# Optimization experiments

Hardware: AMD Instinct MI355X
Metric: run time of the kernel (lower is better)

## Reference

```python
import jax, jax.numpy as jnp
import numpy as np

HIDDEN = 896
N_HEADS = 14
N_KV = 2
HEAD_DIM = HIDDEN // N_HEADS  # 64
N_REP = N_HEADS // N_KV       # 7
ROPE_THETA = 1000000.0


def setup_inputs() -> dict:
    key = jax.random.key(0)
    ks = jax.random.split(key, 8)
    B, S = 2, 2048
    s = 0.02
    return {
        "hidden_states": jax.random.normal(ks[0], (B, S, HIDDEN), dtype=jnp.float32),
        "position_ids": jnp.broadcast_to(jnp.arange(S, dtype=jnp.int64), (B, S)),
        "Wq": jax.random.normal(ks[1], (HIDDEN, HIDDEN), dtype=jnp.float32) * s,
        "bq": jnp.zeros((HIDDEN,), dtype=jnp.float32),
        "Wk": jax.random.normal(ks[2], (N_KV * HEAD_DIM, HIDDEN), dtype=jnp.float32) * s,
        "bk": jnp.zeros((N_KV * HEAD_DIM,), dtype=jnp.float32),
        "Wv": jax.random.normal(ks[3], (N_KV * HEAD_DIM, HIDDEN), dtype=jnp.float32) * s,
        "bv": jnp.zeros((N_KV * HEAD_DIM,), dtype=jnp.float32),
        "Wo": jax.random.normal(ks[4], (HIDDEN, HIDDEN), dtype=jnp.float32) * s,
    }


def _rotate_half(x):
    x1, x2 = x[..., : HEAD_DIM // 2], x[..., HEAD_DIM // 2 :]
    return jnp.concatenate((-x2, x1), axis=-1)


def reference(hidden_states, position_ids, Wq, bq, Wk, bk, Wv, bv, Wo):
    B, S, _ = hidden_states.shape
    q = (hidden_states @ Wq.T + bq).reshape(B, S, N_HEADS, HEAD_DIM)
    k = (hidden_states @ Wk.T + bk).reshape(B, S, N_KV, HEAD_DIM)
    v = (hidden_states @ Wv.T + bv).reshape(B, S, N_KV, HEAD_DIM)

    # RoPE: cos/sin [B, S, 1, HEAD_DIM]
    inv_freq = 1.0 / (ROPE_THETA ** (jnp.arange(0, HEAD_DIM, 2, dtype=jnp.float32) / HEAD_DIM))
    freqs = position_ids.astype(jnp.float32)[..., None] * inv_freq  # [B,S,D/2]
    emb = jnp.concatenate((freqs, freqs), axis=-1)
    cos = jnp.cos(emb)[:, :, None, :]
    sin = jnp.sin(emb)[:, :, None, :]
    q = q * cos + _rotate_half(q) * sin
    k = k * cos + _rotate_half(k) * sin

    # [B, H, S, D]; repeat KV heads (GQA)
    q = q.transpose(0, 2, 1, 3)
    k = jnp.repeat(k.transpose(0, 2, 1, 3), N_REP, axis=1)
    v = jnp.repeat(v.transpose(0, 2, 1, 3), N_REP, axis=1)

    scale = 1.0 / np.sqrt(HEAD_DIM)
    scores = jnp.einsum("bhqd,bhkd->bhqk", q, k) * scale
    causal = jnp.tril(jnp.ones((S, S), dtype=bool))
    scores = jnp.where(causal[None, None, :, :], scores, jnp.finfo(scores.dtype).min)
    probs = jax.nn.softmax(scores, axis=-1)
    attn = jnp.einsum("bhqk,bhkd->bhqd", probs, v)  # [B,H,S,D]
    attn = attn.transpose(0, 2, 1, 3).reshape(B, S, HIDDEN)
    return attn @ Wo.T
```

## Files before the change

kernel.cpp:

```cpp
#include <hip/hip_runtime.h>

#define HID 896
#define NH 14
#define NKV 2
#define NREP 7
#define SEQ 2048
#define BT 2
#define NTOK (BT*SEQ)
#define CSCALE 0.18033688011112042f

typedef __attribute__((ext_vector_type(8))) short bf16x8;
typedef __attribute__((ext_vector_type(8))) unsigned short u16x8;
typedef __attribute__((ext_vector_type(4))) float fx4;
typedef __attribute__((ext_vector_type(4))) short s16x4;
typedef _Float16 f16x4 __attribute__((ext_vector_type(4)));

__device__ __forceinline__ unsigned short f2b(float x){
  union { float f; unsigned u; } a; a.f = x;
  unsigned r = a.u + 0x7FFFu + ((a.u >> 16) & 1u);
  return (unsigned short)(r >> 16);
}
__device__ __forceinline__ unsigned short f2h(float x){
  union { _Float16 h; unsigned short u; } a; a.h = (_Float16)x; return a.u;
}

__global__ __launch_bounds__(256) void qkv_rope_kernel(
    const float* __restrict__ hidden, const int* __restrict__ pos,
    const float* __restrict__ Wq, const float* __restrict__ bq,
    const float* __restrict__ Wk, const float* __restrict__ bk,
    const float* __restrict__ Wv, const float* __restrict__ bv,
    unsigned short* __restrict__ qo, unsigned short* __restrict__ ko,
    unsigned short* __restrict__ vt)
{
  __shared__ short As[64*40];
  __shared__ short Bs[64*40];
  const int tid = threadIdx.x;
  const int bm = blockIdx.x, bn = blockIdx.y;
  const int w = tid >> 6, l = tid & 63, l15 = l & 15, l16 = l >> 4;

  const float *W, *bias; int kind, hloc;
  if (bn < NH)      { W = Wq + (size_t)bn*64*HID;      bias = bq + bn*64;      kind = 0; hloc = bn; }
  else if (bn < 16) { W = Wk + (size_t)(bn-NH)*64*HID; bias = bk + (bn-NH)*64; kind = 1; hloc = bn-NH; }
  else              { W = Wv + (size_t)(bn-16)*64*HID; bias = bv + (bn-16)*64; kind = 2; hloc = bn-16; }

  fx4 acc[4] = {{0,0,0,0},{0,0,0,0},{0,0,0,0},{0,0,0,0}};

  const int r = tid >> 2, c8 = (tid & 3) * 8;
  const float* ap0 = hidden + (size_t)(bm*64 + r)*HID + c8;
  const float* bp0 = W + (size_t)r*HID + c8;

  for (int kc = 0; kc < HID; kc += 32){
    __syncthreads();
    float4 a0 = *(const float4*)(ap0 + kc);
    float4 a1 = *(const float4*)(ap0 + kc + 4);
    float4 b0 = *(const float4*)(bp0 + kc);
    float4 b1 = *(const float4*)(bp0 + kc + 4);
    bf16x8 avv, bvv;
    avv[0]=(short)f2b(a0.x); avv[1]=(short)f2b(a0.y); avv[2]=(short)f2b(a0.z); avv[3]=(short)f2b(a0.w);
    avv[4]=(short)f2b(a1.x); avv[5]=(short)f2b(a1.y); avv[6]=(short)f2b(a1.z); avv[7]=(short)f2b(a1.w);
    bvv[0]=(short)f2b(b0.x); bvv[1]=(short)f2b(b0.y); bvv[2]=(short)f2b(b0.z); bvv[3]=(short)f2b(b0.w);
    bvv[4]=(short)f2b(b1.x); bvv[5]=(short)f2b(b1.y); bvv[6]=(short)f2b(b1.z); bvv[7]=(short)f2b(b1.w);
    *(bf16x8*)&As[r*40 + c8] = avv;
    *(bf16x8*)&Bs[r*40 + c8] = bvv;
    __syncthreads();
    bf16x8 af = *(bf16x8*)&As[(w*16 + l15)*40 + l16*8];
#pragma unroll
    for (int nt = 0; nt < 4; nt++){
      bf16x8 bfr = *(bf16x8*)&Bs[(nt*16 + l15)*40 + l16*8];
      acc[nt] = __builtin_amdgcn_mfma_f32_16x16x32_bf16(af, bfr, acc[nt], 0, 0, 0);
    }
  }

  float bl[4];
#pragma unroll
  for (int nt = 0; nt < 4; nt++) bl[nt] = bias[nt*16 + l15];

  if (kind == 2){
#pragma unroll
    for (int j = 0; j < 4; j++){
      int grow = bm*64 + w*16 + l16*4 + j;
      int b = grow >> 11, s = grow & (SEQ-1);
      int tile = s >> 6, key = s & 63;
      unsigned short* dst = vt + (size_t)(((b*NKV + hloc)*(SEQ/64) + tile)*4096);
#pragma unroll
      for (int nt = 0; nt < 4; nt++)
        dst[(nt*16 + l15)*64 + key] = f2h(acc[nt][j] + bl[nt]);
    }
  } else {
    float invf[2];
#pragma unroll
    for (int nt = 0; nt < 2; nt++)
      invf[nt] = exp2f(-(float)(nt*16 + l15) * 0.62286151779138041f);
#pragma unroll
    for (int j = 0; j < 4; j++){
      int grow = bm*64 + w*16 + l16*4 + j;
      int b = grow >> 11, s = grow & (SEQ-1);
      float p = (float)pos[grow];
      unsigned short* dst = (kind == 0)
          ? qo + ((size_t)(b*NH  + hloc)*SEQ + s)*64
          : ko + ((size_t)(b*NKV + hloc)*SEQ + s)*64;
#pragma unroll
      for (int nt = 0; nt < 2; nt++){
        int d = nt*16 + l15;
        float f = p * invf[nt];
        float sv, cv;
        sincosf(f, &sv, &cv);
        float x1 = acc[nt][j]   + bl[nt];
        float x2 = acc[nt+2][j] + bl[nt+2];
        dst[d]    = f2b(x1*cv - x2*sv);
        dst[d+32] = f2b(x2*cv + x1*sv);
      }
    }
  }
}

__device__ __forceinline__ void smax_pv(
    const fx4* s, bool diag, int wl , int q4,
    float& m_run, float& l_run, fx4* o, const f16x4 vf[4][4])
{
  float tv[16];
#pragma unroll
  for (int tl = 0; tl < 4; tl++)
#pragma unroll
    for (int j = 0; j < 4; j++){
      float x = s[tl][j]*CSCALE;
      if (diag && (tl*16 + q4*4 + j > wl)) x = -1e30f;
      tv[tl*4+j] = x;
    }
  float mx = tv[0];
#pragma unroll
  for (int i = 1; i < 16; i++) mx = fmaxf(mx, tv[i]);
  mx = fmaxf(mx, __shfl_xor(mx, 16));
  mx = fmaxf(mx, __shfl_xor(mx, 32));
  float mn = fmaxf(m_run, mx);
  float al = exp2f(m_run - mn);
  m_run = mn;
  float p[16], rs = 0.f;
#pragma unroll
  for (int i = 0; i < 16; i++){ p[i] = exp2f(tv[i] - mn); rs += p[i]; }
  rs += __shfl_xor(rs, 16);
  rs += __shfl_xor(rs, 32);
  l_run = l_run*al + rs;
#pragma unroll
  for (int nt = 0; nt < 4; nt++)
#pragma unroll
    for (int j = 0; j < 4; j++) o[nt][j] *= al;
  f16x4 pf[4];
#pragma unroll
  for (int tl = 0; tl < 4; tl++){
    pf[tl][0] = (_Float16)p[tl*4+0];
    pf[tl][1] = (_Float16)p[tl*4+1];
    pf[tl][2] = (_Float16)p[tl*4+2];
    pf[tl][3] = (_Float16)p[tl*4+3];
  }
#pragma unroll
  for (int nt = 0; nt < 4; nt++)
#pragma unroll
    for (int tl = 0; tl < 4; tl++)
      o[nt] = __builtin_amdgcn_mfma_f32_16x16x16f16(vf[nt][tl], pf[tl], o[nt], 0,0,0);
}

__global__ __launch_bounds__(256) void attn_kernel(
    const unsigned short* __restrict__ q, const unsigned short* __restrict__ k,
    const unsigned short* __restrict__ vt, unsigned short* __restrict__ ao)
{
  __shared__ short Ks[64*72];
  __shared__ short Vt[64*72];

  const int tid = threadIdx.x;
  const int w = tid >> 6, l = tid & 63, l15 = l & 15, q4 = l >> 4;
  const int tlo = blockIdx.x, thi = 31 - tlo;
  const int h = blockIdx.y, b = blockIdx.z, kvh = h / NREP;
  const int wl = w*16 + l15;

  const unsigned short* qbase = q + ((size_t)(b*NH + h)*SEQ)*64;
  const unsigned short* qpA = qbase + (size_t)(thi*64 + wl)*64;
  const unsigned short* qpB = qbase + (size_t)(tlo*64 + wl)*64;
  bf16x8 qA0 = *(const bf16x8*)(qpA + q4*8), qA1 = *(const bf16x8*)(qpA + 32 + q4*8);
  bf16x8 qB0 = *(const bf16x8*)(qpB + q4*8), qB1 = *(const bf16x8*)(qpB + 32 + q4*8);

  fx4 oA[4] = {{0,0,0,0},{0,0,0,0},{0,0,0,0},{0,0,0,0}};
  fx4 oB[4] = {{0,0,0,0},{0,0,0,0},{0,0,0,0},{0,0,0,0}};
  float mA = -1e30f, lA = 0.f, mB = -1e30f, lB = 0.f;

  const unsigned short* kbase = k  + ((size_t)(b*NKV + kvh)*SEQ)*64;
  const unsigned short* vbase = vt + (size_t)((b*NKV + kvh)*(SEQ/64))*4096;

  u16x8 kreg[2], vreg[2];
#pragma unroll
  for (int p = 0; p < 2; p++){
    int n = p*256 + tid;
    kreg[p] = *(const u16x8*)(kbase + n*8);
    vreg[p] = *(const u16x8*)(vbase + n*8);
  }

  for (int kt = 0; kt <= thi; kt++){
#pragma unroll
    for (int p = 0; p < 2; p++){
      int n = p*256 + tid, rr = n >> 3, g = n & 7;
      *(u16x8*)&Ks[rr*72 + g*8] = kreg[p];
      *(u16x8*)&Vt[rr*72 + g*8] = vreg[p];
    }
    __syncthreads();

    if (kt < thi){
      const unsigned short* kn = kbase + (size_t)(kt+1)*4096;
      const unsigned short* vn = vbase + (size_t)(kt+1)*4096;
#pragma unroll
      for (int p = 0; p < 2; p++){
        int n = p*256 + tid;
        kreg[p] = *(const u16x8*)(kn + n*8);
        vreg[p] = *(const u16x8*)(vn + n*8);
      }
    }

    bf16x8 kf0[4], kf1[4];
#pragma unroll
    for (int tl = 0; tl < 4; tl++){
      kf0[tl] = *(bf16x8*)&Ks[(tl*16 + l15)*72 + q4*8];
      kf1[tl] = *(bf16x8*)&Ks[(tl*16 + l15)*72 + 32 + q4*8];
    }
    f16x4 vf[4][4];
#pragma unroll
    for (int nt = 0; nt < 4; nt++)
#pragma unroll
      for (int tl = 0; tl < 4; tl++)
        vf[nt][tl] = *(f16x4*)&Vt[(nt*16 + l15)*72 + tl*16 + q4*4];

    {
      fx4 s[4] = {{0,0,0,0},{0,0,0,0},{0,0,0,0},{0,0,0,0}};
#pragma unroll
      for (int tl = 0; tl < 4; tl++){
        s[tl] = __builtin_amdgcn_mfma_f32_16x16x32_bf16(kf0[tl], qA0, s[tl], 0,0,0);
        s[tl] = __builtin_amdgcn_mfma_f32_16x16x32_bf16(kf1[tl], qA1, s[tl], 0,0,0);
      }
      smax_pv(s, kt == thi, wl, q4, mA, lA, oA, vf);
    }
    if (kt <= tlo){
      fx4 s[4] = {{0,0,0,0},{0,0,0,0},{0,0,0,0},{0,0,0,0}};
#pragma unroll
      for (int tl = 0; tl < 4; tl++){
        s[tl] = __builtin_amdgcn_mfma_f32_16x16x32_bf16(kf0[tl], qB0, s[tl], 0,0,0);
        s[tl] = __builtin_amdgcn_mfma_f32_16x16x32_bf16(kf1[tl], qB1, s[tl], 0,0,0);
      }
      smax_pv(s, kt == tlo, wl, q4, mB, lB, oB, vf);
    }
    __syncthreads();
  }

  {
    float inv = 1.0f / lA;
    unsigned short* dst = ao + ((size_t)(b*SEQ + thi*64 + wl))*HID + h*64;
#pragma unroll
    for (int nt = 0; nt < 4; nt++){
      s16x4 ov;
      ov[0] = (short)f2b(oA[nt][0]*inv); ov[1] = (short)f2b(oA[nt][1]*inv);
      ov[2] = (short)f2b(oA[nt][2]*inv); ov[3] = (short)f2b(oA[nt][3]*inv);
      *(s16x4*)(dst + nt*16 + q4*4) = ov;
    }
  }
  {
    float inv = 1.0f / lB;
    unsigned short* dst = ao + ((size_t)(b*SEQ + tlo*64 + wl))*HID + h*64;
#pragma unroll
    for (int nt = 0; nt < 4; nt++){
      s16x4 ov;
      ov[0] = (short)f2b(oB[nt][0]*inv); ov[1] = (short)f2b(oB[nt][1]*inv);
      ov[2] = (short)f2b(oB[nt][2]*inv); ov[3] = (short)f2b(oB[nt][3]*inv);
      *(s16x4*)(dst + nt*16 + q4*4) = ov;
    }
  }
}

__global__ __launch_bounds__(256) void out_gemm_kernel(
    const unsigned short* __restrict__ A, const float* __restrict__ Wo,
    float* __restrict__ out)
{
  __shared__ short As[64*40];
  __shared__ short Bs[64*40];
  const int tid = threadIdx.x;
  const int bm = blockIdx.x, bn = blockIdx.y;
  const int w = tid >> 6, l = tid & 63, l15 = l & 15, l16 = l >> 4;

  fx4 acc[4] = {{0,0,0,0},{0,0,0,0},{0,0,0,0},{0,0,0,0}};
  const int r = tid >> 2, c8 = (tid & 3)*8;
  const unsigned short* ap0 = A + (size_t)(bm*64 + r)*HID + c8;
  const float* bp0 = Wo + (size_t)(bn*64 + r)*HID + c8;

  for (int kc = 0; kc < HID; kc += 32){
    __syncthreads();
    u16x8 a8 = *(const u16x8*)(ap0 + kc);
    float4 b0 = *(const float4*)(bp0 + kc);
    float4 b1 = *(const float4*)(bp0 + kc + 4);
    bf16x8 bvv;
    bvv[0]=(short)f2b(b0.x); bvv[1]=(short)f2b(b0.y); bvv[2]=(short)f2b(b0.z); bvv[3]=(short)f2b(b0.w);
    bvv[4]=(short)f2b(b1.x); bvv[5]=(short)f2b(b1.y); bvv[6]=(short)f2b(b1.z); bvv[7]=(short)f2b(b1.w);
    *(u16x8*)&As[r*40 + c8] = a8;
    *(bf16x8*)&Bs[r*40 + c8] = bvv;
    __syncthreads();
    bf16x8 af = *(bf16x8*)&As[(w*16 + l15)*40 + l16*8];
#pragma unroll
    for (int nt = 0; nt < 4; nt++){
      bf16x8 bfr = *(bf16x8*)&Bs[(nt*16 + l15)*40 + l16*8];
      acc[nt] = __builtin_amdgcn_mfma_f32_16x16x32_bf16(af, bfr, acc[nt], 0, 0, 0);
    }
  }

#pragma unroll
  for (int j = 0; j < 4; j++){
    int grow = bm*64 + w*16 + l16*4 + j;
    float* dst = out + (size_t)grow*HID + bn*64;
#pragma unroll
    for (int nt = 0; nt < 4; nt++)
      dst[nt*16 + l15] = acc[nt][j];
  }
}

extern "C" void kernel_launch(void* const* d_in, const int* in_sizes, int n_in,
                              void* d_out, int out_size, void* d_ws, size_t ws_size,
                              hipStream_t stream)
{
  const float* hidden = (const float*)d_in[0];
  const int*   pos    = (const int*)d_in[1];
  const float* Wq = (const float*)d_in[2]; const float* bq = (const float*)d_in[3];
  const float* Wk = (const float*)d_in[4]; const float* bk = (const float*)d_in[5];
  const float* Wv = (const float*)d_in[6]; const float* bv = (const float*)d_in[7];
  const float* Wo = (const float*)d_in[8];

  unsigned short* qws  = (unsigned short*)d_ws;
  unsigned short* kws  = qws + (size_t)BT*NH*SEQ*64;
  unsigned short* vtws = kws + (size_t)BT*NKV*SEQ*64;
  unsigned short* aws  = vtws + (size_t)BT*NKV*SEQ*64;

  qkv_rope_kernel<<<dim3(NTOK/64, 18), 256, 0, stream>>>(
      hidden, pos, Wq, bq, Wk, bk, Wv, bv, qws, kws, vtws);
  attn_kernel<<<dim3(16, NH, BT), 256, 0, stream>>>(qws, kws, vtws, aws);
  out_gemm_kernel<<<dim3(NTOK/64, NH), 256, 0, stream>>>(aws, Wo, (float*)d_out);
}
```

Measured before the change: 186.6 us.

## Pre-convert inputs to bf16 and use 128x128 register-prefetched GEMM tiles

A new conversion kernel turns hidden states and all weights into bf16 once, so the GEMM inner loops no longer repeat the fp32-to-bf16 conversion for every tile. The QKV and output GEMMs move from 64x64 to 128x128 tiles with a 64-wide K step. Each wave now computes a 4x4 grid of MFMA blocks, and the next K tile is prefetched into registers while the current one is computed. The attention output reuses the bf16 hidden-state buffer. In exchange there is an extra kernel launch and extra traffic to write the converted tensors, and the larger tiles leave fewer blocks in the grid, which lowers occupancy.

```diff
diff --git a/kernel.cpp b/kernel.cpp
--- a/kernel.cpp
+++ b/kernel.cpp
@@ -24,98 +24,147 @@
   union { _Float16 h; unsigned short u; } a; a.h = (_Float16)x; return a.u;
 }
 
-__global__ __launch_bounds__(256) void qkv_rope_kernel(
-    const float* __restrict__ hidden, const int* __restrict__ pos,
-    const float* __restrict__ Wq, const float* __restrict__ bq,
-    const float* __restrict__ Wk, const float* __restrict__ bk,
-    const float* __restrict__ Wv, const float* __restrict__ bv,
+__global__ __launch_bounds__(256) void cvt_kernel(
+    const float* __restrict__ s0, const float* __restrict__ s1,
+    const float* __restrict__ s2, const float* __restrict__ s3,
+    const float* __restrict__ s4,
+    unsigned short* __restrict__ d0, unsigned short* __restrict__ d1,
+    unsigned short* __restrict__ d2, unsigned short* __restrict__ d3,
+    unsigned short* __restrict__ d4,
+    int c0, int c1, int c2, int c3, int c4)
+{
+  const float* s; unsigned short* d; int c;
+  switch (blockIdx.y){
+    case 0: s=s0; d=d0; c=c0; break;
+    case 1: s=s1; d=d1; c=c1; break;
+    case 2: s=s2; d=d2; c=c2; break;
+    case 3: s=s3; d=d3; c=c3; break;
+    default: s=s4; d=d4; c=c4; break;
+  }
+  for (int i = (blockIdx.x*256 + threadIdx.x)*8; i < c; i += gridDim.x*2048){
+    float4 a = *(const float4*)(s + i);
+    float4 b = *(const float4*)(s + i + 4);
+    u16x8 o;
+    o[0]=f2b(a.x); o[1]=f2b(a.y); o[2]=f2b(a.z); o[3]=f2b(a.w);
+    o[4]=f2b(b.x); o[5]=f2b(b.y); o[6]=f2b(b.z); o[7]=f2b(b.w);
+    *(u16x8*)(d + i) = o;
+  }
+}
+
+__global__ __launch_bounds__(256) void qkv_gemm_kernel(
+    const unsigned short* __restrict__ A, const unsigned short* __restrict__ Bw,
+    const float* __restrict__ bq, const float* __restrict__ bk, const float* __restrict__ bv,
+    const int* __restrict__ pos,
     unsigned short* __restrict__ qo, unsigned short* __restrict__ ko,
     unsigned short* __restrict__ vt)
 {
-  __shared__ short As[64*40];
-  __shared__ short Bs[64*40];
+  __shared__ short As[128*72];
+  __shared__ short Bs[128*72];
   const int tid = threadIdx.x;
   const int bm = blockIdx.x, bn = blockIdx.y;
-  const int w = tid >> 6, l = tid & 63, l15 = l & 15, l16 = l >> 4;
-
-  const float *W, *bias; int kind, hloc;
-  if (bn < NH)      { W = Wq + (size_t)bn*64*HID;      bias = bq + bn*64;      kind = 0; hloc = bn; }
-  else if (bn < 16) { W = Wk + (size_t)(bn-NH)*64*HID; bias = bk + (bn-NH)*64; kind = 1; hloc = bn-NH; }
-  else              { W = Wv + (size_t)(bn-16)*64*HID; bias = bv + (bn-16)*64; kind = 2; hloc = bn-16; }
-
-  fx4 acc[4] = {{0,0,0,0},{0,0,0,0},{0,0,0,0},{0,0,0,0}};
-
-  const int r = tid >> 2, c8 = (tid & 3) * 8;
-  const float* ap0 = hidden + (size_t)(bm*64 + r)*HID + c8;
-  const float* bp0 = W + (size_t)r*HID + c8;
-
-  for (int kc = 0; kc < HID; kc += 32){
-    __syncthreads();
-    float4 a0 = *(const float4*)(ap0 + kc);
-    float4 a1 = *(const float4*)(ap0 + kc + 4);
-    float4 b0 = *(const float4*)(bp0 + kc);
-    float4 b1 = *(const float4*)(bp0 + kc + 4);
-    bf16x8 avv, bvv;
-    avv[0]=(short)f2b(a0.x); avv[1]=(short)f2b(a0.y); avv[2]=(short)f2b(a0.z); avv[3]=(short)f2b(a0.w);
-    avv[4]=(short)f2b(a1.x); avv[5]=(short)f2b(a1.y); avv[6]=(short)f2b(a1.z); avv[7]=(short)f2b(a1.w);
-    bvv[0]=(short)f2b(b0.x); bvv[1]=(short)f2b(b0.y); bvv[2]=(short)f2b(b0.z); bvv[3]=(short)f2b(b0.w);
-    bvv[4]=(short)f2b(b1.x); bvv[5]=(short)f2b(b1.y); bvv[6]=(short)f2b(b1.z); bvv[7]=(short)f2b(b1.w);
-    *(bf16x8*)&As[r*40 + c8] = avv;
-    *(bf16x8*)&Bs[r*40 + c8] = bvv;
-    __syncthreads();
-    bf16x8 af = *(bf16x8*)&As[(w*16 + l15)*40 + l16*8];
-#pragma unroll
-    for (int nt = 0; nt < 4; nt++){
-      bf16x8 bfr = *(bf16x8*)&Bs[(nt*16 + l15)*40 + l16*8];
-      acc[nt] = __builtin_amdgcn_mfma_f32_16x16x32_bf16(af, bfr, acc[nt], 0, 0, 0);
-    }
-  }
-
+  const int w = tid >> 6, l = tid & 63, l15 = l & 15, q4 = l >> 4;
+  const int wm = w & 1, wn = w >> 1;
+
+  fx4 acc[4][4] = {};
+
+  const int srow = tid >> 3, scol = (tid & 7)*8;
+  const unsigned short* Ag = A  + (size_t)(bm*128 + srow)*HID + scol;
+  const unsigned short* Bg = Bw + (size_t)(bn*128 + srow)*HID + scol;
+
+  u16x8 ar[4], br[4];
+#pragma unroll
+  for (int p = 0; p < 4; p++){
+    ar[p] = *(const u16x8*)(Ag + (size_t)p*32*HID);
+    br[p] = *(const u16x8*)(Bg + (size_t)p*32*HID);
+  }
+
+  for (int kt = 0; kt < 14; kt++){
+#pragma unroll
+    for (int p = 0; p < 4; p++){
+      *(u16x8*)&As[(srow + p*32)*72 + scol] = ar[p];
+      *(u16x8*)&Bs[(srow + p*32)*72 + scol] = br[p];
+    }
+    __syncthreads();
+    if (kt < 13){
+      const int ko_ = (kt+1)*64;
+#pragma unroll
+      for (int p = 0; p < 4; p++){
+        ar[p] = *(const u16x8*)(Ag + (size_t)p*32*HID + ko_);
+        br[p] = *(const u16x8*)(Bg + (size_t)p*32*HID + ko_);
+      }
+    }
+#pragma unroll
+    for (int ks = 0; ks < 2; ks++){
+      bf16x8 af[4], bf[4];
+#pragma unroll
+      for (int mt = 0; mt < 4; mt++)
+        af[mt] = *(bf16x8*)&As[(wm*64 + mt*16 + l15)*72 + ks*32 + q4*8];
+#pragma unroll
+      for (int nt = 0; nt < 4; nt++)
+        bf[nt] = *(bf16x8*)&Bs[(wn*64 + nt*16 + l15)*72 + ks*32 + q4*8];
+#pragma unroll
+      for (int mt = 0; mt < 4; mt++)
+#pragma unroll
+        for (int nt = 0; nt < 4; nt++)
+          acc[mt][nt] = __builtin_amdgcn_mfma_f32_16x16x32_bf16(af[mt], bf[nt], acc[mt][nt], 0,0,0);
+    }
+    __syncthreads();
+  }
+
+  const int hu = bn*2 + wn;
+  const float* bias; int kind, hloc;
+  if (hu < NH)      { bias = bq + hu*64;      kind = 0; hloc = hu; }
+  else if (hu < 16) { bias = bk + (hu-NH)*64; kind = 1; hloc = hu-NH; }
+  else              { bias = bv + (hu-16)*64; kind = 2; hloc = hu-16; }
   float bl[4];
 #pragma unroll
   for (int nt = 0; nt < 4; nt++) bl[nt] = bias[nt*16 + l15];
 
   if (kind == 2){
 #pragma unroll
-    for (int j = 0; j < 4; j++){
-      int grow = bm*64 + w*16 + l16*4 + j;
-      int b = grow >> 11, s = grow & (SEQ-1);
-      int tile = s >> 6, key = s & 63;
-      unsigned short* dst = vt + (size_t)(((b*NKV + hloc)*(SEQ/64) + tile)*4096);
-#pragma unroll
-      for (int nt = 0; nt < 4; nt++)
-        dst[(nt*16 + l15)*64 + key] = f2h(acc[nt][j] + bl[nt]);
-    }
+    for (int mt = 0; mt < 4; mt++)
+#pragma unroll
+      for (int j = 0; j < 4; j++){
+        int grow = bm*128 + wm*64 + mt*16 + q4*4 + j;
+        int b = grow >> 11, s = grow & (SEQ-1);
+        int tile = s >> 6, key = s & 63;
+        unsigned short* dst = vt + (size_t)(((b*NKV + hloc)*(SEQ/64) + tile)*4096);
+#pragma unroll
+        for (int nt = 0; nt < 4; nt++)
+          dst[(nt*16 + l15)*64 + key] = f2h(acc[mt][nt][j] + bl[nt]);
+      }
   } else {
     float invf[2];
 #pragma unroll
     for (int nt = 0; nt < 2; nt++)
       invf[nt] = exp2f(-(float)(nt*16 + l15) * 0.62286151779138041f);
 #pragma unroll
-    for (int j = 0; j < 4; j++){
-      int grow = bm*64 + w*16 + l16*4 + j;
-      int b = grow >> 11, s = grow & (SEQ-1);
-      float p = (float)pos[grow];
-      unsigned short* dst = (kind == 0)
-          ? qo + ((size_t)(b*NH  + hloc)*SEQ + s)*64
-          : ko + ((size_t)(b*NKV + hloc)*SEQ + s)*64;
-#pragma unroll
-      for (int nt = 0; nt < 2; nt++){
-        int d = nt*16 + l15;
-        float f = p * invf[nt];
-        float sv, cv;
-        sincosf(f, &sv, &cv);
-        float x1 = acc[nt][j]   + bl[nt];
-        float x2 = acc[nt+2][j] + bl[nt+2];
-        dst[d]    = f2b(x1*cv - x2*sv);
-        dst[d+32] = f2b(x2*cv + x1*sv);
-      }
-    }
+    for (int mt = 0; mt < 4; mt++)
+#pragma unroll
+      for (int j = 0; j < 4; j++){
+        int grow = bm*128 + wm*64 + mt*16 + q4*4 + j;
+        int b = grow >> 11, s = grow & (SEQ-1);
+        float p = (float)pos[grow];
+        unsigned short* dst = (kind == 0)
+            ? qo + ((size_t)(b*NH  + hloc)*SEQ + s)*64
+            : ko + ((size_t)(b*NKV + hloc)*SEQ + s)*64;
+#pragma unroll
+        for (int nt = 0; nt < 2; nt++){
+          int d = nt*16 + l15;
+          float f = p * invf[nt];
+          float sv, cv;
+          sincosf(f, &sv, &cv);
+          float x1 = acc[mt][nt][j]   + bl[nt];
+          float x2 = acc[mt][nt+2][j] + bl[nt+2];
+          dst[d]    = f2b(x1*cv - x2*sv);
+          dst[d+32] = f2b(x2*cv + x1*sv);
+        }
+      }
   }
 }
 
 __device__ __forceinline__ void smax_pv(
-    const fx4* s, bool diag, int wl , int q4,
+    const fx4* s, bool diag, int wl, int q4,
     float& m_run, float& l_run, fx4* o, const f16x4 vf[4][4])
 {
   float tv[16];
@@ -273,47 +322,72 @@
 }
 
 __global__ __launch_bounds__(256) void out_gemm_kernel(
-    const unsigned short* __restrict__ A, const float* __restrict__ Wo,
+    const unsigned short* __restrict__ A, const unsigned short* __restrict__ Bw,
     float* __restrict__ out)
 {
-  __shared__ short As[64*40];
-  __shared__ short Bs[64*40];
+  __shared__ short As[128*72];
+  __shared__ short Bs[128*72];
   const int tid = threadIdx.x;
   const int bm = blockIdx.x, bn = blockIdx.y;
-  const int w = tid >> 6, l = tid & 63, l15 = l & 15, l16 = l >> 4;
-
-  fx4 acc[4] = {{0,0,0,0},{0,0,0,0},{0,0,0,0},{0,0,0,0}};
-  const int r = tid >> 2, c8 = (tid & 3)*8;
-  const unsigned short* ap0 = A + (size_t)(bm*64 + r)*HID + c8;
-  const float* bp0 = Wo + (size_t)(bn*64 + r)*HID + c8;
-
-  for (int kc = 0; kc < HID; kc += 32){
-    __syncthreads();
-    u16x8 a8 = *(const u16x8*)(ap0 + kc);
-    float4 b0 = *(const float4*)(bp0 + kc);
-    float4 b1 = *(const float4*)(bp0 + kc + 4);
-    bf16x8 bvv;
-    bvv[0]=(short)f2b(b0.x); bvv[1]=(short)f2b(b0.y); bvv[2]=(short)f2b(b0.z); bvv[3]=(short)f2b(b0.w);
-    bvv[4]=(short)f2b(b1.x); bvv[5]=(short)f2b(b1.y); bvv[6]=(short)f2b(b1.z); bvv[7]=(short)f2b(b1.w);
-    *(u16x8*)&As[r*40 + c8] = a8;
-    *(bf16x8*)&Bs[r*40 + c8] = bvv;
-    __syncthreads();
-    bf16x8 af = *(bf16x8*)&As[(w*16 + l15)*40 + l16*8];
-#pragma unroll
-    for (int nt = 0; nt < 4; nt++){
-      bf16x8 bfr = *(bf16x8*)&Bs[(nt*16 + l15)*40 + l16*8];
-      acc[nt] = __builtin_amdgcn_mfma_f32_16x16x32_bf16(af, bfr, acc[nt], 0, 0, 0);
-    }
-  }
-
-#pragma unroll
-  for (int j = 0; j < 4; j++){
-    int grow = bm*64 + w*16 + l16*4 + j;
-    float* dst = out + (size_t)grow*HID + bn*64;
-#pragma unroll
-    for (int nt = 0; nt < 4; nt++)
-      dst[nt*16 + l15] = acc[nt][j];
-  }
+  const int w = tid >> 6, l = tid & 63, l15 = l & 15, q4 = l >> 4;
+  const int wm = w & 1, wn = w >> 1;
+
+  fx4 acc[4][4] = {};
+
+  const int srow = tid >> 3, scol = (tid & 7)*8;
+  const unsigned short* Ag = A  + (size_t)(bm*128 + srow)*HID + scol;
+  const unsigned short* Bg = Bw + (size_t)(bn*128 + srow)*HID + scol;
+
+  u16x8 ar[4], br[4];
+#pragma unroll
+  for (int p = 0; p < 4; p++){
+    ar[p] = *(const u16x8*)(Ag + (size_t)p*32*HID);
+    br[p] = *(const u16x8*)(Bg + (size_t)p*32*HID);
+  }
+
+  for (int kt = 0; kt < 14; kt++){
+#pragma unroll
+    for (int p = 0; p < 4; p++){
+      *(u16x8*)&As[(srow + p*32)*72 + scol] = ar[p];
+      *(u16x8*)&Bs[(srow + p*32)*72 + scol] = br[p];
+    }
+    __syncthreads();
+    if (kt < 13){
+      const int ko_ = (kt+1)*64;
+#pragma unroll
+      for (int p = 0; p < 4; p++){
+        ar[p] = *(const u16x8*)(Ag + (size_t)p*32*HID + ko_);
+        br[p] = *(const u16x8*)(Bg + (size_t)p*32*HID + ko_);
+      }
+    }
+#pragma unroll
+    for (int ks = 0; ks < 2; ks++){
+      bf16x8 af[4], bf[4];
+#pragma unroll
+      for (int mt = 0; mt < 4; mt++)
+        af[mt] = *(bf16x8*)&As[(wm*64 + mt*16 + l15)*72 + ks*32 + q4*8];
+#pragma unroll
+      for (int nt = 0; nt < 4; nt++)
+        bf[nt] = *(bf16x8*)&Bs[(wn*64 + nt*16 + l15)*72 + ks*32 + q4*8];
+#pragma unroll
+      for (int mt = 0; mt < 4; mt++)
+#pragma unroll
+        for (int nt = 0; nt < 4; nt++)
+          acc[mt][nt] = __builtin_amdgcn_mfma_f32_16x16x32_bf16(af[mt], bf[nt], acc[mt][nt], 0,0,0);
+    }
+    __syncthreads();
+  }
+
+#pragma unroll
+  for (int mt = 0; mt < 4; mt++)
+#pragma unroll
+    for (int j = 0; j < 4; j++){
+      int grow = bm*128 + wm*64 + mt*16 + q4*4 + j;
+      float* dst = out + (size_t)grow*HID + bn*128 + wn*64;
+#pragma unroll
+      for (int nt = 0; nt < 4; nt++)
+        dst[nt*16 + l15] = acc[mt][nt][j];
+    }
 }
 
 extern "C" void kernel_launch(void* const* d_in, const int* in_sizes, int n_in,
@@ -327,13 +401,26 @@
   const float* Wv = (const float*)d_in[6]; const float* bv = (const float*)d_in[7];
   const float* Wo = (const float*)d_in[8];
 
-  unsigned short* qws  = (unsigned short*)d_ws;
-  unsigned short* kws  = qws + (size_t)BT*NH*SEQ*64;
-  unsigned short* vtws = kws + (size_t)BT*NKV*SEQ*64;
-  unsigned short* aws  = vtws + (size_t)BT*NKV*SEQ*64;
-
-  qkv_rope_kernel<<<dim3(NTOK/64, 18), 256, 0, stream>>>(
-      hidden, pos, Wq, bq, Wk, bk, Wv, bv, qws, kws, vtws);
-  attn_kernel<<<dim3(16, NH, BT), 256, 0, stream>>>(qws, kws, vtws, aws);
-  out_gemm_kernel<<<dim3(NTOK/64, NH), 256, 0, stream>>>(aws, Wo, (float*)d_out);
-}
+  unsigned short* qws   = (unsigned short*)d_ws;
+  unsigned short* kws   = qws   + (size_t)BT*NH*SEQ*64;
+  unsigned short* vtws  = kws   + (size_t)BT*NKV*SEQ*64;
+  unsigned short* wqkv  = vtws  + (size_t)BT*NKV*SEQ*64;
+  unsigned short* wo16  = wqkv  + (size_t)(NH+2*NKV/2)*0 + 1152*HID;
+  unsigned short* h16   = wo16  + (size_t)HID*HID;
+
+  const int nh   = NTOK*HID;
+  const int nwq  = HID*HID;
+  const int nwkv = 2*64*HID;
+
+  cvt_kernel<<<dim3(448, 5), 256, 0, stream>>>(
+      hidden, Wq, Wk, Wv, Wo,
+      h16, wqkv, wqkv + nwq, wqkv + nwq + nwkv, wo16,
+      nh, nwq, nwkv, nwkv, nwq);
+
+  qkv_gemm_kernel<<<dim3(NTOK/128, 9), 256, 0, stream>>>(
+      h16, wqkv, bq, bk, bv, pos, qws, kws, vtws);
+
+  attn_kernel<<<dim3(16, NH, BT), 256, 0, stream>>>(qws, kws, vtws, h16 );
+
+  out_gemm_kernel<<<dim3(NTOK/128, 7), 256, 0, stream>>>(h16 , wo16, (float*)d_out);
+}
```

Result: faster. 181.6 us (-2.7%).
